# Optimization experiments

Measured on AMD Instinct MI355X. Metric: run time of the kernel, lower is better.

Reference implementation:

```python
import jax, jax.numpy as jnp
import numpy as np

HIDDEN = 1024
NUM_HEADS = 16
HEAD_DIM = HIDDEN // NUM_HEADS  # 64
GRID_SIZE = 5
SPLINE_ORDER = 3
GRID_LO, GRID_HI = -1.0, 1.0


def b_splines(x2d, grid, k=SPLINE_ORDER):
    # x2d: (N, in), grid: (in, GRID_SIZE + 2k + 1) -> (N, in, GRID_SIZE + k)
    xg = x2d[:, :, None]
    g = grid[None, :, :]
    bases = ((xg >= g[:, :, :-1]) & (xg < g[:, :, 1:])).astype(x2d.dtype)
    for j in range(1, k + 1):
        left = (xg - g[:, :, : -(j + 1)]) / (g[:, :, j:-1] - g[:, :, : -(j + 1)]) * bases[:, :, :-1]
        right = (g[:, :, j + 1 :] - xg) / (g[:, :, j + 1 :] - g[:, :, 1:-j]) * bases[:, :, 1:]
        bases = left + right
    return bases


def setup_inputs() -> dict:
    key = jax.random.key(0)
    ks = jax.random.split(key, 6)
    B, S = 1, 2048
    in_f, out_f = HIDDEN, 3 * HIDDEN
    x = jax.random.normal(ks[0], (B, S, HIDDEN), dtype=jnp.float32)
    base_weight = jax.random.normal(ks[1], (out_f, in_f), dtype=jnp.float32) * (1.0 / np.sqrt(in_f))
    n_coef = GRID_SIZE + SPLINE_ORDER  # 8
    spline_weight = jax.random.normal(ks[2], (out_f, in_f, n_coef), dtype=jnp.float32) * 0.1
    spline_scaler = jnp.ones((out_f, in_f), dtype=jnp.float32)
    out_w = jax.random.normal(ks[3], (HIDDEN, HIDDEN), dtype=jnp.float32) * (1.0 / np.sqrt(HIDDEN))
    out_b = jnp.zeros((HIDDEN,), dtype=jnp.float32)
    # extended B-spline grid, same for every input feature
    h = (GRID_HI - GRID_LO) / GRID_SIZE
    grid_row = jnp.arange(-SPLINE_ORDER, GRID_SIZE + SPLINE_ORDER + 1, dtype=jnp.float32) * h + GRID_LO
    grid = jnp.tile(grid_row[None, :], (in_f, 1))  # (in, GRID_SIZE + 2k + 1)
    # RoPE rotation matrix (cos/sin of pos * theta), theta base 10000
    half = HEAD_DIM // 2
    inv_freq = 1.0 / (10000.0 ** (jnp.arange(0, half, dtype=jnp.float32) / half))
    angles = jnp.arange(S, dtype=jnp.float32)[:, None] * inv_freq[None, :]  # (S, half)
    rot_cos = jnp.cos(angles)
    rot_sin = jnp.sin(angles)
    return {"x": x, "base_weight": base_weight, "spline_weight": spline_weight,
            "spline_scaler": spline_scaler, "out_w": out_w, "out_b": out_b,
            "grid": grid, "rot_cos": rot_cos, "rot_sin": rot_sin}


def apply_rope(t, rot_cos, rot_sin):
    # t: (B, H, S, D); pairs (t[..., 2i], t[..., 2i+1]) viewed as complex, mult by cis
    tr = t[..., 0::2]
    ti = t[..., 1::2]
    c = rot_cos[None, None, :, :]
    s = rot_sin[None, None, :, :]
    nr = tr * c - ti * s
    ni = tr * s + ti * c
    return jnp.stack([nr, ni], axis=-1).reshape(t.shape)


def reference(x, base_weight, spline_weight, spline_scaler, out_w, out_b, grid, rot_cos, rot_sin):
    B, S, H = x.shape
    N = B * S
    x2 = x.reshape(N, H)
    # KANLinear: base branch + spline branch
    base = jax.nn.silu(x2) @ base_weight.T  # (N, 3H)
    bs = b_splines(x2, grid)  # (N, in, G+k)
    sw = (spline_weight * spline_scaler[:, :, None]).reshape(spline_weight.shape[0], -1)
    spline = bs.reshape(N, -1) @ sw.T
    qkv = (base + spline).reshape(B, S, NUM_HEADS, 3 * HEAD_DIM).transpose(0, 2, 1, 3)
    q, k, v = jnp.split(qkv, 3, axis=-1)  # each (B, nh, S, hd)
    q = apply_rope(q, rot_cos, rot_sin)
    k = apply_rope(k, rot_cos, rot_sin)
    scores = jnp.einsum("bhqd,bhkd->bhqk", q, k) / np.sqrt(HEAD_DIM).astype(np.float32)
    attn = jax.nn.softmax(scores, axis=-1)
    ctx = jnp.einsum("bhqk,bhkd->bhqd", attn, v)
    ctx = ctx.transpose(0, 2, 1, 3).reshape(B, S, H)
    return ctx @ out_w.T + out_b
```

## Files before the change

### kernel.cpp

```cpp
#include <hip/hip_runtime.h>

#define DEVI __device__ __forceinline__

typedef float f32x4 __attribute__((ext_vector_type(4)));
typedef __bf16 bf16x8 __attribute__((ext_vector_type(8)));

constexpr int S   = 2048;
constexpr int HID = 1024;
constexpr int HD  = 64;
constexpr int O3  = 3072;
constexpr int KF  = 9216;

DEVI unsigned short f2bf(float f) {
  unsigned int u = __float_as_uint(f);
  u = (u + 0x7FFFu + ((u >> 16) & 1u)) >> 16;
  return (unsigned short)u;
}
DEVI float b2f(unsigned int u) { return __uint_as_float(u << 16); }
DEVI float fexp(float x) { return __builtin_amdgcn_exp2f(x * 1.44269504089f); }

DEVI void gload16(const void* g, void* l) {
  __builtin_amdgcn_global_load_lds((const __attribute__((address_space(1))) void*)g,
                                   (__attribute__((address_space(3))) void*)l, 16, 0, 0);
}

__global__ __launch_bounds__(256) void kconv_w(const float* __restrict__ bw,
    const float* __restrict__ sw, const float* __restrict__ sc,
    unsigned short* __restrict__ Wc) {
  unsigned int t = blockIdx.x * 256 + threadIdx.x;
  unsigned int o = t / 1152, jc = t % 1152;
  unsigned int j = jc * 8;
  float v[8];
  if (j < 1024) {
    const float4* p = (const float4*)(bw + (size_t)o * 1024 + j);
    float4 a = p[0], b = p[1];
    v[0]=a.x; v[1]=a.y; v[2]=a.z; v[3]=a.w; v[4]=b.x; v[5]=b.y; v[6]=b.z; v[7]=b.w;
  } else {
    unsigned int i = (j - 1024) >> 3;
    float s = sc[(size_t)o * 1024 + i];
    const float4* p = (const float4*)(sw + ((size_t)o * 1024 + i) * 8);
    float4 a = p[0], b = p[1];
    v[0]=a.x*s; v[1]=a.y*s; v[2]=a.z*s; v[3]=a.w*s; v[4]=b.x*s; v[5]=b.y*s; v[6]=b.z*s; v[7]=b.w*s;
  }
  union { unsigned short u[8]; uint4 q; } pk;
  #pragma unroll
  for (int c = 0; c < 8; ++c) pk.u[c] = f2bf(v[c]);
  *(uint4*)(Wc + (size_t)o * KF + j) = pk.q;
}

__global__ __launch_bounds__(256) void kconv_outw(const float* __restrict__ ow,
    unsigned short* __restrict__ Wo) {
  unsigned int t = blockIdx.x * 256 + threadIdx.x;
  unsigned int o = t >> 7, j = (t & 127) * 8;
  const float4* p = (const float4*)(ow + (size_t)o * 1024 + j);
  float4 a = p[0], b = p[1];
  float v[8] = {a.x, a.y, a.z, a.w, b.x, b.y, b.z, b.w};
  union { unsigned short u[8]; uint4 q; } pk;
  #pragma unroll
  for (int c = 0; c < 8; ++c) pk.u[c] = f2bf(v[c]);
  *(uint4*)(Wo + (size_t)o * 1024 + j) = pk.q;
}

__global__ __launch_bounds__(256) void kfeatures(const float* __restrict__ x,
    const float* __restrict__ grid, unsigned short* __restrict__ F) {
  unsigned int t = blockIdx.x * 256 + threadIdx.x;
  unsigned int n = t >> 10, i = t & 1023;
  float xv = x[t];
  float sil = xv / (1.f + expf(-xv));
  F[(size_t)n * KF + i] = f2bf(sil);
  float g[12];
  #pragma unroll
  for (int j = 0; j < 12; ++j) g[j] = grid[j];
  float b[11];
  #pragma unroll
  for (int j = 0; j < 11; ++j) b[j] = (xv >= g[j] && xv < g[j + 1]) ? 1.f : 0.f;
  #pragma unroll
  for (int ord = 1; ord <= 3; ++ord) {
    float inv[11];
    #pragma unroll
    for (int a = 0; a + ord < 12 && a < 11; ++a) {
      float d = g[a + ord] - g[a];
      float r = __builtin_amdgcn_rcpf(d);
      inv[a] = r * (2.f - d * r);
    }
    #pragma unroll
    for (int j = 0; j + ord < 11; ++j)
      b[j] = (xv - g[j]) * inv[j] * b[j]
           + (g[j + ord + 1] - xv) * inv[j + 1] * b[j + 1];
  }
  union { unsigned short u[8]; uint4 q; } pk;
  #pragma unroll
  for (int c = 0; c < 8; ++c) pk.u[c] = f2bf(b[c]);
  *(uint4*)(F + (size_t)n * KF + 1024 + i * 8) = pk.q;
}

__global__ __launch_bounds__(256) void kgemm_bt(const unsigned short* __restrict__ A,
    const unsigned short* __restrict__ W, void* __restrict__ C,
    const float* __restrict__ bias, int N, int nkPer, int mode) {
  int bm, bn, kz;
  if (mode == 1) {
    int gxy = gridDim.x * gridDim.y;
    int nwg = gxy * gridDim.z;
    int lin = blockIdx.x + gridDim.x * (blockIdx.y + gridDim.y * blockIdx.z);
    int per = nwg >> 3;
    int swz = (lin & 7) * per + (lin >> 3);
    kz = swz / gxy;
    int r = swz - kz * gxy;
    bm = r / gridDim.y;
    bn = r - bm * gridDim.y;
  } else { bm = blockIdx.x; bn = blockIdx.y; kz = 0; }
  const int tid = threadIdx.x;
  const int w = tid >> 6, lane = tid & 63;
  const int l16 = lane & 15, g4 = lane >> 4;
  const int wr = w >> 1, wc = w & 1;
  __shared__ __align__(16) unsigned short As[2][128 * 32];
  __shared__ __align__(16) unsigned short Bs[2][128 * 32];
  f32x4 acc[4][4] = {};
  const int K = (mode == 1) ? KF : 1024;
  const int koff = kz * nkPer;

  auto STAGE = [&](int buf, int kt) {
    #pragma unroll
    for (int r = 0; r < 2; ++r) {
      int chunk = r * 256 + w * 64 + lane;
      int row = chunk >> 2, col = (chunk & 3) * 8;
      int ldsoff = (r * 256 + w * 64) * 16;
      gload16(A + (size_t)(bm * 128 + row) * K + kt * 32 + col, (char*)As[buf] + ldsoff);
      gload16(W + (size_t)(bn * 128 + row) * K + kt * 32 + col, (char*)Bs[buf] + ldsoff);
    }
  };

  STAGE(0, koff);
  asm volatile("s_waitcnt vmcnt(0)" ::: "memory");
  __syncthreads();
  int cur = 0;
  for (int kt = koff; kt < koff + nkPer; ++kt) {
    if (kt + 1 < koff + nkPer) STAGE(cur ^ 1, kt + 1);
    bf16x8 af[4], bfr[4];
    #pragma unroll
    for (int f = 0; f < 4; ++f)
      af[f] = *(const bf16x8*)(As[cur] + (wr * 64 + f * 16 + l16) * 32 + g4 * 8);
    #pragma unroll
    for (int f = 0; f < 4; ++f)
      bfr[f] = *(const bf16x8*)(Bs[cur] + (wc * 64 + f * 16 + l16) * 32 + g4 * 8);
    __builtin_amdgcn_s_setprio(1);
    #pragma unroll
    for (int fr = 0; fr < 4; ++fr)
      #pragma unroll
      for (int fc = 0; fc < 4; ++fc)
        acc[fr][fc] = __builtin_amdgcn_mfma_f32_16x16x32_bf16(af[fr], bfr[fc], acc[fr][fc], 0, 0, 0);
    __builtin_amdgcn_s_setprio(0);
    asm volatile("s_waitcnt vmcnt(0)" ::: "memory");
    __syncthreads();
    cur ^= 1;
  }
  if (mode == 0) {
    float* Cf = (float*)C;
    #pragma unroll
    for (int fr = 0; fr < 4; ++fr) {
      int rowb = bm * 128 + wr * 64 + fr * 16 + g4 * 4;
      #pragma unroll
      for (int fc = 0; fc < 4; ++fc) {
        int col = bn * 128 + wc * 64 + fc * 16 + l16;
        float bv = bias[col];
        #pragma unroll
        for (int rg = 0; rg < 4; ++rg)
          Cf[(size_t)(rowb + rg) * N + col] = acc[fr][fc][rg] + bv;
      }
    }
  } else {
    unsigned short* Cb = (unsigned short*)C + (size_t)kz * 2048 * N;
    #pragma unroll
    for (int fr = 0; fr < 4; ++fr) {
      int rowb = bm * 128 + wr * 64 + fr * 16 + g4 * 4;
      #pragma unroll
      for (int fc = 0; fc < 4; ++fc) {
        int col = bn * 128 + wc * 64 + fc * 16 + l16;
        #pragma unroll
        for (int rg = 0; rg < 4; ++rg)
          Cb[(size_t)(rowb + rg) * N + col] = f2bf(acc[fr][fc][rg]);
      }
    }
  }
}

__global__ __launch_bounds__(256) void krope_qk(const unsigned short* __restrict__ qp,
    int splits, const float* __restrict__ rc, const float* __restrict__ rs,
    unsigned short* __restrict__ Qb, unsigned short* __restrict__ Kb) {
  unsigned int t = blockIdx.x * 256 + threadIdx.x;
  int d = t & 31;
  int h = (t >> 5) & 15;
  int n = t >> 9;
  float qr = 0.f, qi = 0.f, kr = 0.f, ki = 0.f;
  for (int p = 0; p < splits; ++p) {
    size_t base = (size_t)p * 2048 * O3 + (size_t)n * O3 + h * 192;
    unsigned int a = *(const unsigned int*)(qp + base + 2 * d);
    unsigned int e = *(const unsigned int*)(qp + base + 64 + 2 * d);
    qr += b2f(a & 0xffffu); qi += b2f(a >> 16);
    kr += b2f(e & 0xffffu); ki += b2f(e >> 16);
  }
  float c = rc[n * 32 + d], sn = rs[n * 32 + d];
  unsigned int qpk = (unsigned int)f2bf((qr * c - qi * sn) * 0.125f)
                   | ((unsigned int)f2bf((qr * sn + qi * c) * 0.125f) << 16);
  unsigned int kpk = (unsigned int)f2bf(kr * c - ki * sn)
                   | ((unsigned int)f2bf(kr * sn + ki * c) << 16);
  *(unsigned int*)(Qb + (size_t)h * S * HD + (size_t)n * HD + 2 * d) = qpk;
  *(unsigned int*)(Kb + (size_t)h * S * HD + (size_t)n * HD + 2 * d) = kpk;
}

__global__ __launch_bounds__(256) void kpack_vt(const unsigned short* __restrict__ qp,
    int splits, unsigned short* __restrict__ Vt) {
  const int nt = blockIdx.x;
  const int h  = blockIdx.y;
  const int tid = threadIdx.x;
  __shared__ __align__(16) unsigned short T[64][72];
  const int n0 = nt * 64;
  #pragma unroll
  for (int it = 0; it < 2; ++it) {
    int idx = it * 256 + tid;
    int r = idx >> 3;
    int c8 = (idx & 7) * 8;
    float acc[8] = {};
    for (int p = 0; p < splits; ++p) {
      size_t base = (size_t)p * 2048 * O3 + (size_t)(n0 + r) * O3 + h * 192 + 128 + c8;
      uint4 u = *(const uint4*)(qp + base);
      const unsigned short* pu = (const unsigned short*)&u;
      #pragma unroll
      for (int j = 0; j < 8; ++j) acc[j] += b2f(pu[j]);
    }
    #pragma unroll
    for (int j = 0; j < 8; ++j) T[c8 + j][r] = f2bf(acc[j]);
  }
  __syncthreads();
  #pragma unroll
  for (int it = 0; it < 2; ++it) {
    int idx = it * 256 + tid;
    int dd = idx >> 3;
    int c8 = (idx & 7) * 8;
    *(uint4*)(Vt + (size_t)h * HD * S + (size_t)dd * S + n0 + c8) = *(const uint4*)&T[dd][c8];
  }
}

__global__ __launch_bounds__(256) void kattn(const unsigned short* __restrict__ Qb,
    const unsigned short* __restrict__ Kb, const unsigned short* __restrict__ Vt,
    unsigned short* __restrict__ ctx) {
  const int qb = blockIdx.x, h = blockIdx.y;
  const int tid = threadIdx.x, w = tid >> 6, lane = tid & 63;
  const int l16 = lane & 15, g4 = lane >> 4;
  __shared__ __align__(16) unsigned short Ks[2][64 * 64];
  __shared__ __align__(16) unsigned short Vs[2][64 * 64];
  __shared__ __align__(16) unsigned short Ps[4][16 * 64];
  const unsigned short* Qh = Qb + (size_t)h * S * HD;
  const unsigned short* Kh = Kb + (size_t)h * S * HD;
  const unsigned short* Vh = Vt + (size_t)h * HD * S;
  bf16x8 qf[2];
  #pragma unroll
  for (int ks = 0; ks < 2; ++ks)
    qf[ks] = *(const bf16x8*)(Qh + (size_t)(qb * 64 + w * 16 + l16) * HD + ks * 32 + g4 * 8);
  f32x4 o[4] = {};
  float lp[4] = {0.f, 0.f, 0.f, 0.f};

  auto STAGE = [&](int buf, int t) {
    int kv0 = t * 64;
    #pragma unroll
    for (int r = 0; r < 2; ++r) {
      int chunk = r * 256 + w * 64 + lane;
      int row = chunk >> 3;
      int c8 = ((chunk ^ row) & 7) * 8;
      int ldsoff = (r * 256 + w * 64) * 16;
      gload16(Kh + (size_t)(kv0 + row) * HD + c8, (char*)Ks[buf] + ldsoff);
      gload16(Vh + (size_t)row * S + kv0 + c8, (char*)Vs[buf] + ldsoff);
    }
  };

  STAGE(0, 0);
  asm volatile("s_waitcnt vmcnt(0)" ::: "memory");
  __syncthreads();
  int cur = 0;
  for (int t = 0; t < S / 64; ++t) {
    if (t + 1 < S / 64) STAGE(cur ^ 1, t + 1);
    const unsigned short* Kc = Ks[cur];
    const unsigned short* Vc = Vs[cur];
    f32x4 s[4] = {};
    __builtin_amdgcn_s_setprio(1);
    #pragma unroll
    for (int fc = 0; fc < 4; ++fc) {
      int rw = fc * 16 + l16;
      #pragma unroll
      for (int ks = 0; ks < 2; ++ks) {
        bf16x8 bk = *(const bf16x8*)(Kc + rw * 64 + (((ks * 4 + g4) ^ (l16 & 7)) * 8));
        s[fc] = __builtin_amdgcn_mfma_f32_16x16x32_bf16(qf[ks], bk, s[fc], 0, 0, 0);
      }
    }
    __builtin_amdgcn_s_setprio(0);
    #pragma unroll
    for (int fc = 0; fc < 4; ++fc)
      #pragma unroll
      for (int rg = 0; rg < 4; ++rg) {
        float p = fexp(s[fc][rg]);
        lp[rg] += p;
        int row = g4 * 4 + rg;
        Ps[w][row * 64 + ((fc * 2 + (l16 >> 3)) ^ (row & 7)) * 8 + (l16 & 7)] = f2bf(p);
      }
    __builtin_amdgcn_s_setprio(1);
    #pragma unroll
    for (int ks = 0; ks < 2; ++ks) {
      bf16x8 ap = *(const bf16x8*)(Ps[w] + l16 * 64 + (((ks * 4 + g4) ^ (l16 & 7)) * 8));
      #pragma unroll
      for (int fc = 0; fc < 4; ++fc) {
        int rw = fc * 16 + l16;
        bf16x8 bv = *(const bf16x8*)(Vc + rw * 64 + (((ks * 4 + g4) ^ (l16 & 7)) * 8));
        o[fc] = __builtin_amdgcn_mfma_f32_16x16x32_bf16(ap, bv, o[fc], 0, 0, 0);
      }
    }
    __builtin_amdgcn_s_setprio(0);
    asm volatile("s_waitcnt vmcnt(0)" ::: "memory");
    __syncthreads();
    cur ^= 1;
  }
  #pragma unroll
  for (int rg = 0; rg < 4; ++rg) {
    float l = lp[rg];
    l += __shfl_xor(l, 1, 64);
    l += __shfl_xor(l, 2, 64);
    l += __shfl_xor(l, 4, 64);
    l += __shfl_xor(l, 8, 64);
    float inv = 1.f / l;
    int row = qb * 64 + w * 16 + g4 * 4 + rg;
    #pragma unroll
    for (int fc = 0; fc < 4; ++fc)
      ctx[(size_t)row * HID + h * HD + fc * 16 + l16] = f2bf(o[fc][rg] * inv);
  }
}

extern "C" void kernel_launch(void* const* d_in, const int* in_sizes, int n_in,
                              void* d_out, int out_size, void* d_ws, size_t ws_size,
                              hipStream_t stream) {
  const float* x    = (const float*)d_in[0];
  const float* bw   = (const float*)d_in[1];
  const float* sw   = (const float*)d_in[2];
  const float* sc   = (const float*)d_in[3];
  const float* ow   = (const float*)d_in[4];
  const float* ob   = (const float*)d_in[5];
  const float* grid = (const float*)d_in[6];
  const float* rc   = (const float*)d_in[7];
  const float* rs   = (const float*)d_in[8];
  float* out = (float*)d_out;
  char* ws = (char*)d_ws;

  const size_t PARTIAL = (size_t)2048 * O3 * 2;
  int splits = (ws_size >= (size_t)96468992 + 4 * PARTIAL + 4 * 4194304) ? 4 : 2;

  unsigned short* F    = (unsigned short*)(ws);
  unsigned short* Wc   = (unsigned short*)(ws + 37748736);
  unsigned short* Wo   = (unsigned short*)(ws + 94371840);
  unsigned short* qkvp = (unsigned short*)(ws + 96468992);
  char* tail = ws + 96468992 + (size_t)splits * PARTIAL;
  unsigned short* Qb   = (unsigned short*)(tail);
  unsigned short* Kb   = (unsigned short*)(tail + 4194304);
  unsigned short* Vt   = (unsigned short*)(tail + 8388608);
  unsigned short* ctx  = (unsigned short*)(tail + 12582912);

  kconv_w   <<<dim3(13824), dim3(256), 0, stream>>>(bw, sw, sc, Wc);
  kconv_outw<<<dim3(512),   dim3(256), 0, stream>>>(ow, Wo);
  kfeatures <<<dim3(8192),  dim3(256), 0, stream>>>(x, grid, F);
  kgemm_bt  <<<dim3(16, 24, splits), dim3(256), 0, stream>>>(F, Wc, qkvp, (const float*)nullptr, 3072, 288 / splits, 1);
  krope_qk  <<<dim3(4096),  dim3(256), 0, stream>>>(qkvp, splits, rc, rs, Qb, Kb);
  kpack_vt  <<<dim3(32, 16), dim3(256), 0, stream>>>(qkvp, splits, Vt);
  kattn     <<<dim3(32, 16), dim3(256), 0, stream>>>(Qb, Kb, Vt, ctx);
  kgemm_bt  <<<dim3(16, 8, 1),  dim3(256), 0, stream>>>(ctx, Wo, out, ob, 1024, 32, 0);
}
```

Baseline: 421.6 us.

## Replace split-K KAN GEMM with 256x192-tile, 8-wave pipelined kernel

```diff
diff --git a/kernel.cpp b/kernel.cpp
--- a/kernel.cpp
+++ b/kernel.cpp
@@ -23,6 +23,10 @@
   __builtin_amdgcn_global_load_lds((const __attribute__((address_space(1))) void*)g,
                                    (__attribute__((address_space(3))) void*)l, 16, 0, 0);
 }
+
+#define BAR() asm volatile("s_barrier" ::: "memory")
+#define VMC0() asm volatile("s_waitcnt vmcnt(0)" ::: "memory")
+#define VMC2() asm volatile("s_waitcnt vmcnt(2)" ::: "memory")
 
 __global__ __launch_bounds__(256) void kconv_w(const float* __restrict__ bw,
     const float* __restrict__ sw, const float* __restrict__ sc,
@@ -94,30 +98,125 @@
   *(uint4*)(F + (size_t)n * KF + 1024 + i * 8) = pk.q;
 }
 
+__global__ __launch_bounds__(512) void kgemm256(const unsigned short* __restrict__ A,
+    const unsigned short* __restrict__ W, unsigned short* __restrict__ C) {
+  int lin = blockIdx.x + (blockIdx.y << 3) + (blockIdx.z << 7);
+  int swz = (lin & 7) * 32 + (lin >> 3);
+  int kz = swz >> 7;
+  int r = swz & 127;
+  int bm = r >> 4, bn = r & 15;
+  const int tid = threadIdx.x;
+  const int wid = tid >> 6;
+  const int lane = tid & 63;
+  const int l16 = lane & 15, g4 = lane >> 4;
+  const int wr = wid >> 2, wc = wid & 3;
+  const int koff = kz * 72;
+
+  __shared__ __align__(16) unsigned short As[2][2][128 * 64];
+  __shared__ __align__(16) unsigned short Bs[2][192 * 64];
+
+  const size_t rA0 = (size_t)bm * 256;
+  const size_t rB0 = (size_t)bn * 192;
+
+  auto stageA = [&](int buf, int half, int t) {
+    const unsigned short* src = A + (rA0 + half * 128) * (size_t)KF + (size_t)(koff + t) * 64;
+    char* lds = (char*)As[buf][half];
+    #pragma unroll
+    for (int rr = 0; rr < 2; ++rr) {
+      int chunk = rr * 512 + tid;
+      int row = chunk >> 3;
+      int c8 = (chunk & 7) ^ (row & 7);
+      gload16(src + (size_t)row * KF + c8 * 8, lds + (rr * 512 + wid * 64) * 16);
+    }
+  };
+  auto stageB = [&](int buf, int third, int t) {
+    const unsigned short* src = W + (rB0 + third * 64) * (size_t)KF + (size_t)(koff + t) * 64;
+    char* lds = (char*)Bs[buf] + third * 8192;
+    int row = tid >> 3;
+    int c8 = (tid & 7) ^ (row & 7);
+    gload16(src + (size_t)row * KF + c8 * 8, lds + (wid * 64) * 16);
+  };
+
+  f32x4 acc[8][3] = {};
+  bf16x8 bb[3][2];
+
+#define GPH(Q, BUF, STMTS, DOVM) do {                                          \
+    bf16x8 ar[2][2];                                                           \
+    _Pragma("unroll") for (int f = 0; f < 2; ++f)                              \
+      _Pragma("unroll") for (int ks = 0; ks < 2; ++ks) {                       \
+        int rw = (2 * (Q) + f) * 16 + l16;                                     \
+        ar[f][ks] = *(const bf16x8*)(As[BUF][wr] + rw * 64 +                   \
+                                     (((ks * 4 + g4) ^ (l16 & 7)) * 8));       \
+      }                                                                        \
+    if ((Q) == 0) {                                                            \
+      _Pragma("unroll") for (int fb = 0; fb < 3; ++fb)                         \
+        _Pragma("unroll") for (int ks = 0; ks < 2; ++ks) {                     \
+          int rw = wc * 48 + fb * 16 + l16;                                    \
+          bb[fb][ks] = *(const bf16x8*)(Bs[BUF] + rw * 64 +                    \
+                                        (((ks * 4 + g4) ^ (l16 & 7)) * 8));    \
+        }                                                                      \
+    }                                                                          \
+    STMTS;                                                                     \
+    if (DOVM) VMC2();                                                          \
+    BAR();                                                                     \
+    __builtin_amdgcn_s_setprio(1);                                             \
+    _Pragma("unroll") for (int f = 0; f < 2; ++f)                              \
+      _Pragma("unroll") for (int fb = 0; fb < 3; ++fb)                         \
+        _Pragma("unroll") for (int ks = 0; ks < 2; ++ks)                       \
+          acc[2 * (Q) + f][fb] = __builtin_amdgcn_mfma_f32_16x16x32_bf16(      \
+              ar[f][ks], bb[fb][ks], acc[2 * (Q) + f][fb], 0, 0, 0);           \
+    __builtin_amdgcn_s_setprio(0);                                             \
+    BAR();                                                                     \
+  } while (0)
+
+  stageB(0, 0, 0); stageB(0, 1, 0); stageB(0, 2, 0);
+  stageA(0, 0, 0); stageA(0, 1, 0);
+  stageB(1, 0, 1); stageB(1, 1, 1); stageB(1, 2, 1);
+  VMC0();
+  BAR();
+
+  for (int it = 0; it < 36; ++it) {
+    int t0 = 2 * it;
+    int tA1 = t0 + 1;
+    int tN0 = t0 + 2 < 72 ? t0 + 2 : 71;
+    int tN1 = t0 + 3 < 72 ? t0 + 3 : 71;
+    GPH(0, 0, { stageA(1, 0, tA1); }, 0);
+    GPH(1, 0, { stageA(1, 1, tA1); stageB(0, 0, tN0); }, 0);
+    GPH(2, 0, { stageB(0, 1, tN0); }, 0);
+    GPH(3, 0, { stageB(0, 2, tN0); }, 1);
+    GPH(0, 1, { stageA(0, 0, tN0); }, 0);
+    GPH(1, 1, { stageA(0, 1, tN0); stageB(1, 0, tN1); }, 0);
+    GPH(2, 1, { stageB(1, 1, tN1); }, 0);
+    GPH(3, 1, { stageB(1, 2, tN1); }, 1);
+  }
+#undef GPH
+
+  unsigned short* Cb = C + (size_t)kz * 2048 * 3072;
+  #pragma unroll
+  for (int fr = 0; fr < 8; ++fr) {
+    int rowb = bm * 256 + wr * 128 + fr * 16 + g4 * 4;
+    #pragma unroll
+    for (int fb = 0; fb < 3; ++fb) {
+      int col = bn * 192 + wc * 48 + fb * 16 + l16;
+      #pragma unroll
+      for (int rg = 0; rg < 4; ++rg)
+        Cb[(size_t)(rowb + rg) * 3072 + col] = f2bf(acc[fr][fb][rg]);
+    }
+  }
+}
+
 __global__ __launch_bounds__(256) void kgemm_bt(const unsigned short* __restrict__ A,
-    const unsigned short* __restrict__ W, void* __restrict__ C,
-    const float* __restrict__ bias, int N, int nkPer, int mode) {
-  int bm, bn, kz;
-  if (mode == 1) {
-    int gxy = gridDim.x * gridDim.y;
-    int nwg = gxy * gridDim.z;
-    int lin = blockIdx.x + gridDim.x * (blockIdx.y + gridDim.y * blockIdx.z);
-    int per = nwg >> 3;
-    int swz = (lin & 7) * per + (lin >> 3);
-    kz = swz / gxy;
-    int r = swz - kz * gxy;
-    bm = r / gridDim.y;
-    bn = r - bm * gridDim.y;
-  } else { bm = blockIdx.x; bn = blockIdx.y; kz = 0; }
+    const unsigned short* __restrict__ W, float* __restrict__ C,
+    const float* __restrict__ bias, int N, int nkPer) {
+  const int bm = blockIdx.x, bn = blockIdx.y;
   const int tid = threadIdx.x;
   const int w = tid >> 6, lane = tid & 63;
   const int l16 = lane & 15, g4 = lane >> 4;
-  const int wr = w >> 1, wc = w & 1;
+  const int wr = w >> 1, wcc = w & 1;
   __shared__ __align__(16) unsigned short As[2][128 * 32];
   __shared__ __align__(16) unsigned short Bs[2][128 * 32];
   f32x4 acc[4][4] = {};
-  const int K = (mode == 1) ? KF : 1024;
-  const int koff = kz * nkPer;
+  const int K = 1024;
 
   auto STAGE = [&](int buf, int kt) {
     #pragma unroll
@@ -130,19 +229,19 @@
     }
   };
 
-  STAGE(0, koff);
-  asm volatile("s_waitcnt vmcnt(0)" ::: "memory");
-  __syncthreads();
+  STAGE(0, 0);
+  VMC0();
+  BAR();
   int cur = 0;
-  for (int kt = koff; kt < koff + nkPer; ++kt) {
-    if (kt + 1 < koff + nkPer) STAGE(cur ^ 1, kt + 1);
+  for (int kt = 0; kt < nkPer; ++kt) {
+    if (kt + 1 < nkPer) STAGE(cur ^ 1, kt + 1);
     bf16x8 af[4], bfr[4];
     #pragma unroll
     for (int f = 0; f < 4; ++f)
       af[f] = *(const bf16x8*)(As[cur] + (wr * 64 + f * 16 + l16) * 32 + g4 * 8);
     #pragma unroll
     for (int f = 0; f < 4; ++f)
-      bfr[f] = *(const bf16x8*)(Bs[cur] + (wc * 64 + f * 16 + l16) * 32 + g4 * 8);
+      bfr[f] = *(const bf16x8*)(Bs[cur] + (wcc * 64 + f * 16 + l16) * 32 + g4 * 8);
     __builtin_amdgcn_s_setprio(1);
     #pragma unroll
     for (int fr = 0; fr < 4; ++fr)
@@ -150,36 +249,20 @@
       for (int fc = 0; fc < 4; ++fc)
         acc[fr][fc] = __builtin_amdgcn_mfma_f32_16x16x32_bf16(af[fr], bfr[fc], acc[fr][fc], 0, 0, 0);
     __builtin_amdgcn_s_setprio(0);
-    asm volatile("s_waitcnt vmcnt(0)" ::: "memory");
-    __syncthreads();
+    VMC0();
+    BAR();
     cur ^= 1;
   }
-  if (mode == 0) {
-    float* Cf = (float*)C;
-    #pragma unroll
-    for (int fr = 0; fr < 4; ++fr) {
-      int rowb = bm * 128 + wr * 64 + fr * 16 + g4 * 4;
-      #pragma unroll
-      for (int fc = 0; fc < 4; ++fc) {
-        int col = bn * 128 + wc * 64 + fc * 16 + l16;
-        float bv = bias[col];
-        #pragma unroll
-        for (int rg = 0; rg < 4; ++rg)
-          Cf[(size_t)(rowb + rg) * N + col] = acc[fr][fc][rg] + bv;
-      }
-    }
-  } else {
-    unsigned short* Cb = (unsigned short*)C + (size_t)kz * 2048 * N;
-    #pragma unroll
-    for (int fr = 0; fr < 4; ++fr) {
-      int rowb = bm * 128 + wr * 64 + fr * 16 + g4 * 4;
-      #pragma unroll
-      for (int fc = 0; fc < 4; ++fc) {
-        int col = bn * 128 + wc * 64 + fc * 16 + l16;
-        #pragma unroll
-        for (int rg = 0; rg < 4; ++rg)
-          Cb[(size_t)(rowb + rg) * N + col] = f2bf(acc[fr][fc][rg]);
-      }
+  #pragma unroll
+  for (int fr = 0; fr < 4; ++fr) {
+    int rowb = bm * 128 + wr * 64 + fr * 16 + g4 * 4;
+    #pragma unroll
+    for (int fc = 0; fc < 4; ++fc) {
+      int col = bn * 128 + wcc * 64 + fc * 16 + l16;
+      float bv = bias[col];
+      #pragma unroll
+      for (int rg = 0; rg < 4; ++rg)
+        C[(size_t)(rowb + rg) * N + col] = acc[fr][fc][rg] + bv;
     }
   }
 }
@@ -274,8 +357,8 @@
   };
 
   STAGE(0, 0);
-  asm volatile("s_waitcnt vmcnt(0)" ::: "memory");
-  __syncthreads();
+  VMC0();
+  BAR();
   int cur = 0;
   for (int t = 0; t < S / 64; ++t) {
     if (t + 1 < S / 64) STAGE(cur ^ 1, t + 1);
@@ -314,8 +397,8 @@
       }
     }
     __builtin_amdgcn_s_setprio(0);
-    asm volatile("s_waitcnt vmcnt(0)" ::: "memory");
-    __syncthreads();
+    VMC0();
+    BAR();
     cur ^= 1;
   }
   #pragma unroll
@@ -348,14 +431,13 @@
   float* out = (float*)d_out;
   char* ws = (char*)d_ws;
 
-  const size_t PARTIAL = (size_t)2048 * O3 * 2;
-  int splits = (ws_size >= (size_t)96468992 + 4 * PARTIAL + 4 * 4194304) ? 4 : 2;
+  const int splits = 2;
 
   unsigned short* F    = (unsigned short*)(ws);
   unsigned short* Wc   = (unsigned short*)(ws + 37748736);
   unsigned short* Wo   = (unsigned short*)(ws + 94371840);
   unsigned short* qkvp = (unsigned short*)(ws + 96468992);
-  char* tail = ws + 96468992 + (size_t)splits * PARTIAL;
+  char* tail = ws + 96468992 + (size_t)splits * 12582912;
   unsigned short* Qb   = (unsigned short*)(tail);
   unsigned short* Kb   = (unsigned short*)(tail + 4194304);
   unsigned short* Vt   = (unsigned short*)(tail + 8388608);
@@ -364,9 +446,9 @@
   kconv_w   <<<dim3(13824), dim3(256), 0, stream>>>(bw, sw, sc, Wc);
   kconv_outw<<<dim3(512),   dim3(256), 0, stream>>>(ow, Wo);
   kfeatures <<<dim3(8192),  dim3(256), 0, stream>>>(x, grid, F);
-  kgemm_bt  <<<dim3(16, 24, splits), dim3(256), 0, stream>>>(F, Wc, qkvp, (const float*)nullptr, 3072, 288 / splits, 1);
+  kgemm256  <<<dim3(8, 16, 2), dim3(512), 0, stream>>>(F, Wc, qkvp);
   krope_qk  <<<dim3(4096),  dim3(256), 0, stream>>>(qkvp, splits, rc, rs, Qb, Kb);
   kpack_vt  <<<dim3(32, 16), dim3(256), 0, stream>>>(qkvp, splits, Vt);
   kattn     <<<dim3(32, 16), dim3(256), 0, stream>>>(Qb, Kb, Vt, ctx);
-  kgemm_bt  <<<dim3(16, 8, 1),  dim3(256), 0, stream>>>(ctx, Wo, out, ob, 1024, 32, 0);
-}
+  kgemm_bt  <<<dim3(16, 8),  dim3(256), 0, stream>>>(ctx, Wo, out, ob, 1024, 32);
+}
```

Measured after the change: 421.6 us. No clear change (+0.0%).
